# Optimization experiments

Measured on AMD Instinct MI355X. Metric: run time of the kernel, lower is better.

## Reference

```python
import jax, jax.numpy as jnp
import numpy as np

VERY_NEG = -1e30


def setup_inputs() -> dict:
    key = jax.random.key(0)
    k1, k2, k3, k4, k5 = jax.random.split(key, 5)
    T, J, B, D = 1024, 128, 32, 256
    context = jax.random.normal(k1, (T, B, D), dtype=jnp.float32)
    question = jax.random.normal(k2, (J, B, D), dtype=jnp.float32)
    con_lens = jax.random.randint(k3, (B,), 1, T + 1)
    qu_lens = jax.random.randint(k4, (B,), 1, J + 1)
    # learned trilinear weight (3*D, 1), small init like uniform weight init
    att_w = jax.random.normal(k5, (3 * D, 1), dtype=jnp.float32) * 0.05
    return {"context": context, "question": question, "con_lens": con_lens,
            "qu_lens": qu_lens, "att_w": att_w}


def reference(context, question, con_lens, qu_lens, att_w):
    T, B, D = context.shape
    J = question.shape[0]
    # Decompose trilinear score: [c, q, c*q] @ att_w = c.w_c + q.w_q + (c*q).w_cq
    w_c, w_q, w_cq = att_w[:D, 0], att_w[D:2 * D, 0], att_w[2 * D:, 0]
    c_proj = jnp.einsum('tbd,d->bt', context, w_c)            # (B,T)
    q_proj = jnp.einsum('jbd,d->bj', question, w_q)           # (B,J)
    cross = jnp.einsum('tbd,jbd->btj', context * w_cq, question)  # (B,T,J)
    S = c_proj[:, :, None] + q_proj[:, None, :] + cross       # (B,T,J)
    # exp_mask: valid (t < con_len) & (j < qu_len), invalid += VERY_NEG
    t_valid = jnp.arange(T)[None, :] < con_lens[:, None]      # (B,T)
    j_valid = jnp.arange(J)[None, :] < qu_lens[:, None]       # (B,J)
    valid = t_valid[:, :, None] & j_valid[:, None, :]         # (B,T,J)
    S = S + jnp.where(valid, 0.0, VERY_NEG)
    # context-to-query attention
    c2q_w = jax.nn.softmax(S, axis=-1)                        # (B,T,J)
    question_bt = jnp.transpose(question, (1, 0, 2))          # (B,J,D)
    c2q = jnp.einsum('btj,bjd->btd', c2q_w, question_bt)      # (B,T,D)
    # query-to-context attention: rows of the expanded bmm are identical,
    # so compute the weighted sum once and broadcast (same math as expand+bmm)
    value = jax.nn.softmax(jnp.max(S, axis=2), axis=-1)       # (B,T)
    context_bt = jnp.transpose(context, (1, 0, 2))            # (B,T,D)
    q2c_vec = jnp.einsum('bt,btd->bd', value, context_bt)     # (B,D)
    q2c = jnp.broadcast_to(q2c_vec[:, None, :], (B, T, D))
    G = jnp.concatenate([context_bt, c2q, context_bt * c2q, context_bt * q2c],
                        axis=2)                               # (B,T,4D)
    # zero out padded context positions
    G = G * t_valid[:, :, None].astype(G.dtype)
    return G
```

## Files before the change

kernel.cpp:

```cpp
#include <hip/hip_runtime.h>
#include <hip/hip_bf16.h>

#define T_ 1024
#define J_ 128
#define B_ 32
#define D_ 256
#define VERY_NEG (-1e30f)

using u16 = unsigned short;
typedef __bf16 bf16x8 __attribute__((ext_vector_type(8)));
typedef u16 u16x4 __attribute__((ext_vector_type(4)));
typedef float f32x4 __attribute__((ext_vector_type(4)));

__device__ __forceinline__ float bf2f(u16 u) {
  union { unsigned int i; float f; } v; v.i = ((unsigned int)u) << 16; return v.f;
}
__device__ __forceinline__ u16 f2bf(float f) {
  union { float f; unsigned int i; } v; v.f = f;
  unsigned int i = v.i;
  return (u16)((i + 0x7fffu + ((i >> 16) & 1u)) >> 16);
}

__global__ __launch_bounds__(256) void k_qproj(const float* __restrict__ qst,
                                               const float* __restrict__ attw,
                                               float* __restrict__ ws_qproj) {
  const int wave = threadIdx.x >> 6, lane = threadIdx.x & 63;
  const int gid = blockIdx.x * 4 + wave;
  const int b = gid >> 7, j = gid & 127;
  const float* src = qst + (size_t)j * (B_ * D_) + b * D_ + lane * 4;
  f32x4 a = *(const f32x4*)src;
  f32x4 w = *(const f32x4*)(attw + D_ + lane * 4);
  float s = a[0] * w[0] + a[1] * w[1] + a[2] * w[2] + a[3] * w[3];
#pragma unroll
  for (int m = 32; m >= 1; m >>= 1) s += __shfl_xor(s, m);
  if (lane == 0) ws_qproj[gid] = s;
}

__global__ __launch_bounds__(256) void k_main(const float* __restrict__ ctx,
                                              const float* __restrict__ qst,
                                              const int* __restrict__ con_lens,
                                              const int* __restrict__ qu_lens,
                                              const float* __restrict__ attw,
                                              const float* __restrict__ ws_qproj,
                                              float* __restrict__ ws_mrow,
                                              float* __restrict__ out) {
  __shared__ __align__(16) u16 smem[24576];
  u16* qtl = smem;
  u16* plds = smem + 16384;
  u16* c2q_l = smem;

  const int tid = threadIdx.x;
  const int wave = tid >> 6, lane = tid & 63;
  const int lrow = lane & 15, lgrp = lane >> 4;
  const int b = blockIdx.y;
  const int t0 = blockIdx.x * 64;
  const int t0w = t0 + wave * 16;
  const int con = con_lens[b], qu = qu_lens[b];

  f32x4 accS[8];
#pragma unroll
  for (int jb = 0; jb < 8; ++jb) accS[jb] = f32x4{0.f, 0.f, 0.f, 0.f};

  float cpr = 0.f;
  const float* rowAp = ctx + (size_t)(t0w + lrow) * (B_ * D_) + b * D_;
#pragma unroll
  for (int ks = 0; ks < 8; ++ks) {
    const int d0 = ks * 32 + lgrp * 8;
    f32x4 a0 = *(const f32x4*)(rowAp + d0);
    f32x4 a1 = *(const f32x4*)(rowAp + d0 + 4);
    f32x4 wq0 = *(const f32x4*)(attw + 2 * D_ + d0);
    f32x4 wq1 = *(const f32x4*)(attw + 2 * D_ + d0 + 4);
    f32x4 wc0 = *(const f32x4*)(attw + d0);
    f32x4 wc1 = *(const f32x4*)(attw + d0 + 4);
    bf16x8 afrag;
#pragma unroll
    for (int e = 0; e < 4; ++e) {
      afrag[e] = (__bf16)(a0[e] * wq0[e]);
      afrag[4 + e] = (__bf16)(a1[e] * wq1[e]);
      cpr += a0[e] * wc0[e] + a1[e] * wc1[e];
    }
#pragma unroll
    for (int jb = 0; jb < 8; ++jb) {
      const float* rb = qst + (size_t)(jb * 16 + lrow) * (B_ * D_) + b * D_ + d0;
      f32x4 b0 = *(const f32x4*)(rb);
      f32x4 b1 = *(const f32x4*)(rb + 4);
      bf16x8 bfrag;
#pragma unroll
      for (int e = 0; e < 4; ++e) {
        bfrag[e] = (__bf16)b0[e];
        bfrag[4 + e] = (__bf16)b1[e];
      }
      accS[jb] = __builtin_amdgcn_mfma_f32_16x16x32_bf16(afrag, bfrag, accS[jb], 0, 0, 0);
    }
  }
  cpr += __shfl_xor(cpr, 16);
  cpr += __shfl_xor(cpr, 32);

  float cp[4];
#pragma unroll
  for (int r = 0; r < 4; ++r) cp[r] = __shfl(cpr, lgrp * 4 + r);
  float qp[8];
#pragma unroll
  for (int jb = 0; jb < 8; ++jb) qp[jb] = ws_qproj[b * 128 + jb * 16 + lrow];

  float mx[4] = {-3e38f, -3e38f, -3e38f, -3e38f};
#pragma unroll
  for (int jb = 0; jb < 8; ++jb) {
    const int j = jb * 16 + lrow;
#pragma unroll
    for (int r = 0; r < 4; ++r) {
      const int t = t0w + lgrp * 4 + r;
      float s = accS[jb][r] + cp[r] + qp[jb];
      if (t >= con || j >= qu) s += VERY_NEG;
      accS[jb][r] = s;
      mx[r] = fmaxf(mx[r], s);
    }
  }
#pragma unroll
  for (int r = 0; r < 4; ++r) {
    mx[r] = fmaxf(mx[r], __shfl_xor(mx[r], 1));
    mx[r] = fmaxf(mx[r], __shfl_xor(mx[r], 2));
    mx[r] = fmaxf(mx[r], __shfl_xor(mx[r], 4));
    mx[r] = fmaxf(mx[r], __shfl_xor(mx[r], 8));
  }
  if (lrow == 0) {
#pragma unroll
    for (int r = 0; r < 4; ++r) ws_mrow[b * 1024 + t0w + lgrp * 4 + r] = mx[r];
  }
  float sm[4] = {0.f, 0.f, 0.f, 0.f};
#pragma unroll
  for (int jb = 0; jb < 8; ++jb)
#pragma unroll
    for (int r = 0; r < 4; ++r) {
      float p = __expf(accS[jb][r] - mx[r]);
      accS[jb][r] = p;
      sm[r] += p;
    }
#pragma unroll
  for (int r = 0; r < 4; ++r) {
    sm[r] += __shfl_xor(sm[r], 1);
    sm[r] += __shfl_xor(sm[r], 2);
    sm[r] += __shfl_xor(sm[r], 4);
    sm[r] += __shfl_xor(sm[r], 8);
  }

  {
    u16* pl = plds + wave * 2048;
#pragma unroll
    for (int r = 0; r < 4; ++r) {
      const float inv = 1.0f / sm[r];
      const int m = lgrp * 4 + r;
#pragma unroll
      for (int jb = 0; jb < 8; ++jb) {
        const int n = jb * 16 + lrow;
        pl[m * 128 + (((n >> 3) ^ m) << 3) + (n & 7)] = f2bf(accS[jb][r] * inv);
      }
    }
  }

  f32x4 accO[16];
#pragma unroll
  for (int nb = 0; nb < 16; ++nb) accO[nb] = f32x4{0.f, 0.f, 0.f, 0.f};

#pragma unroll
  for (int h = 0; h < 2; ++h) {
    __syncthreads();
    for (int it = 0; it < 8; ++it) {
      const int task = it * 256 + tid;
      const int j = task & 127, dblk = task >> 7;
      const float* qp8 = qst + (size_t)j * (B_ * D_) + b * D_ + h * 128 + dblk * 8;
      f32x4 q0 = *(const f32x4*)(qp8);
      f32x4 q1 = *(const f32x4*)(qp8 + 4);
#pragma unroll
      for (int e = 0; e < 8; ++e) {
        const int dl = dblk * 8 + e;
        const float v = (e < 4) ? q0[e] : q1[e - 4];
        qtl[dl * 128 + (((j >> 3) ^ (dl & 15)) << 3) + (j & 7)] = f2bf(v);
      }
    }
    __syncthreads();
#pragma unroll
    for (int ks2 = 0; ks2 < 4; ++ks2) {
      const int chunkA = ks2 * 4 + lgrp;
      const bf16x8 ap =
          *(const bf16x8*)(plds + wave * 2048 + lrow * 128 + ((chunkA ^ lrow) << 3));
#pragma unroll
      for (int nbl = 0; nbl < 8; ++nbl) {
        const int dl = nbl * 16 + lrow;
        const bf16x8 bq = *(const bf16x8*)(qtl + dl * 128 + ((chunkA ^ (dl & 15)) << 3));
        accO[h * 8 + nbl] =
            __builtin_amdgcn_mfma_f32_16x16x32_bf16(ap, bq, accO[h * 8 + nbl], 0, 0, 0);
      }
    }
  }
  __syncthreads();

#pragma unroll
  for (int nb = 0; nb < 16; ++nb)
#pragma unroll
    for (int r = 0; r < 4; ++r) {
      const int row = wave * 16 + lgrp * 4 + r;
      const int d = nb * 16 + lrow;
      c2q_l[row * 264 + d] = f2bf(accO[nb][r]);
    }
  __syncthreads();

  for (int ii = 0; ii < 16; ++ii) {
    const int idx = ii * 256 + tid;
    const int row = idx >> 6, c = idx & 63;
    const int t = t0 + row;
    const bool valid = t < con;
    f32x4 cr = *(const f32x4*)(ctx + (size_t)t * (B_ * D_) + b * D_ + c * 4);
    u16x4 cq = *(const u16x4*)(c2q_l + row * 264 + c * 4);
    f32x4 p0, p1, p2;
#pragma unroll
    for (int e = 0; e < 4; ++e) {
      const float cf = valid ? cr[e] : 0.f;
      const float qf = valid ? bf2f(cq[e]) : 0.f;
      p0[e] = cf;
      p1[e] = qf;
      p2[e] = cf * qf;
    }
    float* g = out + ((size_t)(b * 1024 + t)) * 1024 + c * 4;
    *(f32x4*)(g) = p0;
    *(f32x4*)(g + 256) = p1;
    *(f32x4*)(g + 512) = p2;
  }
}

__global__ __launch_bounds__(256) void k_value(const float* __restrict__ ctx,
                                               const float* __restrict__ mrow,
                                               float* __restrict__ q2c) {
  __shared__ float wls[1024];
  __shared__ float red[8];
  const int b = blockIdx.x >> 3, tc = blockIdx.x & 7;
  const int tid = threadIdx.x;
  const int wave = tid >> 6, lane = tid & 63;
  const float* mr = mrow + b * 1024;

  float mx = -3e38f;
  for (int t = tid; t < 1024; t += 256) mx = fmaxf(mx, mr[t]);
#pragma unroll
  for (int m = 32; m >= 1; m >>= 1) mx = fmaxf(mx, __shfl_xor(mx, m));
  if (lane == 0) red[wave] = mx;
  __syncthreads();
  mx = fmaxf(fmaxf(red[0], red[1]), fmaxf(red[2], red[3]));

  float sl = 0.f;
  for (int t = tid; t < 1024; t += 256) {
    float wv = __expf(mr[t] - mx);
    wls[t] = wv;
    sl += wv;
  }
#pragma unroll
  for (int m = 32; m >= 1; m >>= 1) sl += __shfl_xor(sl, m);
  if (lane == 0) red[4 + wave] = sl;
  __syncthreads();
  const float inv = 1.0f / (red[4] + red[5] + red[6] + red[7]);

  const int d = tid;
  const float* cp = ctx + b * D_ + d;
  const int tb = tc * 128;
  float a0 = 0.f, a1 = 0.f, a2 = 0.f, a3 = 0.f;
  for (int t = tb; t < tb + 128; t += 4) {
    a0 += wls[t + 0] * cp[(size_t)(t + 0) * (B_ * D_)];
    a1 += wls[t + 1] * cp[(size_t)(t + 1) * (B_ * D_)];
    a2 += wls[t + 2] * cp[(size_t)(t + 2) * (B_ * D_)];
    a3 += wls[t + 3] * cp[(size_t)(t + 3) * (B_ * D_)];
  }
  atomicAdd(&q2c[b * D_ + d], (a0 + a1 + a2 + a3) * inv);
}

__global__ __launch_bounds__(256) void k_part3(const float* __restrict__ ctx,
                                               const int* __restrict__ con_lens,
                                               const float* __restrict__ q2c,
                                               float* __restrict__ out) {
  const int idx = blockIdx.x * 256 + threadIdx.x;
  const int c = idx & 63, t = (idx >> 6) & 1023, b = idx >> 16;
  const bool valid = t < con_lens[b];
  f32x4 cr = *(const f32x4*)(ctx + (size_t)t * (B_ * D_) + b * D_ + c * 4);
  const f32x4 qv = *(const f32x4*)(q2c + b * D_ + c * 4);
  f32x4 o;
#pragma unroll
  for (int e = 0; e < 4; ++e) o[e] = valid ? cr[e] * qv[e] : 0.f;
  *(f32x4*)(out + ((size_t)(b * 1024 + t)) * 1024 + 768 + c * 4) = o;
}

extern "C" void kernel_launch(void* const* d_in, const int* in_sizes, int n_in,
                              void* d_out, int out_size, void* d_ws, size_t ws_size,
                              hipStream_t stream) {
  const float* ctx = (const float*)d_in[0];
  const float* qst = (const float*)d_in[1];
  const int* con = (const int*)d_in[2];
  const int* qu = (const int*)d_in[3];
  const float* attw = (const float*)d_in[4];
  float* out = (float*)d_out;

  float* ws = (float*)d_ws;
  float* ws_qproj = ws;
  float* ws_mrow = ws + 4096;
  float* ws_q2c = ws + 36864;

  hipMemsetAsync((void*)ws_q2c, 0, B_ * D_ * sizeof(float), stream);
  k_qproj<<<1024, 256, 0, stream>>>(qst, attw, ws_qproj);
  k_main<<<dim3(16, 32), 256, 0, stream>>>(ctx, qst, con, qu, attw, ws_qproj, ws_mrow,
                                           out);
  k_value<<<256, 256, 0, stream>>>(ctx, ws_mrow, ws_q2c);
  k_part3<<<8192, 256, 0, stream>>>(ctx, con, ws_q2c, out);
}
```

Measured before the change: 218.9 us.

## Fuse q2c softmax partials into main kernel and precast question to bf16

```diff
diff --git a/kernel.cpp b/kernel.cpp
--- a/kernel.cpp
+++ b/kernel.cpp
@@ -9,6 +9,7 @@
 
 using u16 = unsigned short;
 typedef __bf16 bf16x8 __attribute__((ext_vector_type(8)));
+typedef u16 u16x8 __attribute__((ext_vector_type(8)));
 typedef u16 u16x4 __attribute__((ext_vector_type(4)));
 typedef float f32x4 __attribute__((ext_vector_type(4)));
 
@@ -21,15 +22,20 @@
   return (u16)((i + 0x7fffu + ((i >> 16) & 1u)) >> 16);
 }
 
-__global__ __launch_bounds__(256) void k_qproj(const float* __restrict__ qst,
-                                               const float* __restrict__ attw,
-                                               float* __restrict__ ws_qproj) {
+__global__ __launch_bounds__(256) void k_prep(const float* __restrict__ qst,
+                                              const float* __restrict__ attw,
+                                              float* __restrict__ ws_qproj,
+                                              u16* __restrict__ ws_qbf) {
   const int wave = threadIdx.x >> 6, lane = threadIdx.x & 63;
   const int gid = blockIdx.x * 4 + wave;
   const int b = gid >> 7, j = gid & 127;
-  const float* src = qst + (size_t)j * (B_ * D_) + b * D_ + lane * 4;
-  f32x4 a = *(const f32x4*)src;
+  const size_t off = (size_t)j * (B_ * D_) + b * D_ + lane * 4;
+  f32x4 a = *(const f32x4*)(qst + off);
   f32x4 w = *(const f32x4*)(attw + D_ + lane * 4);
+  u16x4 qb;
+#pragma unroll
+  for (int e = 0; e < 4; ++e) qb[e] = f2bf(a[e]);
+  *(u16x4*)(ws_qbf + off) = qb;
   float s = a[0] * w[0] + a[1] * w[1] + a[2] * w[2] + a[3] * w[3];
 #pragma unroll
   for (int m = 32; m >= 1; m >>= 1) s += __shfl_xor(s, m);
@@ -37,17 +43,22 @@
 }
 
 __global__ __launch_bounds__(256) void k_main(const float* __restrict__ ctx,
-                                              const float* __restrict__ qst,
+                                              const u16* __restrict__ qbf,
                                               const int* __restrict__ con_lens,
                                               const int* __restrict__ qu_lens,
                                               const float* __restrict__ attw,
                                               const float* __restrict__ ws_qproj,
-                                              float* __restrict__ ws_mrow,
+                                              float* __restrict__ ws_mtile,
+                                              float* __restrict__ ws_pden,
+                                              float* __restrict__ ws_pnum,
                                               float* __restrict__ out) {
   __shared__ __align__(16) u16 smem[24576];
+  __shared__ float mrow_l[64];
+  __shared__ float msc[1];
   u16* qtl = smem;
   u16* plds = smem + 16384;
   u16* c2q_l = smem;
+  float* red4 = (float*)(smem + 16896);
 
   const int tid = threadIdx.x;
   const int wave = tid >> 6, lane = tid & 63;
@@ -81,15 +92,8 @@
     }
 #pragma unroll
     for (int jb = 0; jb < 8; ++jb) {
-      const float* rb = qst + (size_t)(jb * 16 + lrow) * (B_ * D_) + b * D_ + d0;
-      f32x4 b0 = *(const f32x4*)(rb);
-      f32x4 b1 = *(const f32x4*)(rb + 4);
-      bf16x8 bfrag;
-#pragma unroll
-      for (int e = 0; e < 4; ++e) {
-        bfrag[e] = (__bf16)b0[e];
-        bfrag[4 + e] = (__bf16)b1[e];
-      }
+      const bf16x8 bfrag =
+          *(const bf16x8*)(qbf + (size_t)(jb * 16 + lrow) * (B_ * D_) + b * D_ + d0);
       accS[jb] = __builtin_amdgcn_mfma_f32_16x16x32_bf16(afrag, bfrag, accS[jb], 0, 0, 0);
     }
   }
@@ -125,7 +129,7 @@
   }
   if (lrow == 0) {
 #pragma unroll
-    for (int r = 0; r < 4; ++r) ws_mrow[b * 1024 + t0w + lgrp * 4 + r] = mx[r];
+    for (int r = 0; r < 4; ++r) mrow_l[wave * 16 + lgrp * 4 + r] = mx[r];
   }
   float sm[4] = {0.f, 0.f, 0.f, 0.f};
 #pragma unroll
@@ -168,14 +172,11 @@
     for (int it = 0; it < 8; ++it) {
       const int task = it * 256 + tid;
       const int j = task & 127, dblk = task >> 7;
-      const float* qp8 = qst + (size_t)j * (B_ * D_) + b * D_ + h * 128 + dblk * 8;
-      f32x4 q0 = *(const f32x4*)(qp8);
-      f32x4 q1 = *(const f32x4*)(qp8 + 4);
+      u16x8 q = *(const u16x8*)(qbf + (size_t)j * (B_ * D_) + b * D_ + h * 128 + dblk * 8);
 #pragma unroll
       for (int e = 0; e < 8; ++e) {
         const int dl = dblk * 8 + e;
-        const float v = (e < 4) ? q0[e] : q1[e - 4];
-        qtl[dl * 128 + (((j >> 3) ^ (dl & 15)) << 3) + (j & 7)] = f2bf(v);
+        qtl[dl * 128 + (((j >> 3) ^ (dl & 15)) << 3) + (j & 7)] = q[e];
       }
     }
     __syncthreads();
@@ -205,13 +206,37 @@
     }
   __syncthreads();
 
+  if (tid < 64) {
+    float v = mrow_l[tid];
+#pragma unroll
+    for (int m = 32; m >= 1; m >>= 1) v = fmaxf(v, __shfl_xor(v, m));
+    if (tid == 0) msc[0] = v;
+  }
+  __syncthreads();
+  const float Mt = msc[0];
+  if (tid < 64) {
+    const float mr = mrow_l[tid];
+    const float e = (mr < -1e29f) ? 0.f : __expf(mr - Mt);
+    mrow_l[tid] = e;
+    float s2 = e;
+#pragma unroll
+    for (int m = 32; m >= 1; m >>= 1) s2 += __shfl_xor(s2, m);
+    if (tid == 0) {
+      ws_mtile[b * 16 + blockIdx.x] = Mt;
+      ws_pden[b * 16 + blockIdx.x] = s2;
+    }
+  }
+  __syncthreads();
+
+  f32x4 acc4 = {0.f, 0.f, 0.f, 0.f};
+  const int c = tid & 63;
   for (int ii = 0; ii < 16; ++ii) {
-    const int idx = ii * 256 + tid;
-    const int row = idx >> 6, c = idx & 63;
+    const int row = ii * 4 + wave;
     const int t = t0 + row;
     const bool valid = t < con;
     f32x4 cr = *(const f32x4*)(ctx + (size_t)t * (B_ * D_) + b * D_ + c * 4);
     u16x4 cq = *(const u16x4*)(c2q_l + row * 264 + c * 4);
+    const float w = mrow_l[row];
     f32x4 p0, p1, p2;
 #pragma unroll
     for (int e = 0; e < 4; ++e) {
@@ -220,55 +245,47 @@
       p0[e] = cf;
       p1[e] = qf;
       p2[e] = cf * qf;
+      acc4[e] += w * cr[e];
     }
     float* g = out + ((size_t)(b * 1024 + t)) * 1024 + c * 4;
     *(f32x4*)(g) = p0;
     *(f32x4*)(g + 256) = p1;
     *(f32x4*)(g + 512) = p2;
   }
-}
-
-__global__ __launch_bounds__(256) void k_value(const float* __restrict__ ctx,
-                                               const float* __restrict__ mrow,
-                                               float* __restrict__ q2c) {
-  __shared__ float wls[1024];
-  __shared__ float red[8];
-  const int b = blockIdx.x >> 3, tc = blockIdx.x & 7;
-  const int tid = threadIdx.x;
-  const int wave = tid >> 6, lane = tid & 63;
-  const float* mr = mrow + b * 1024;
-
-  float mx = -3e38f;
-  for (int t = tid; t < 1024; t += 256) mx = fmaxf(mx, mr[t]);
-#pragma unroll
-  for (int m = 32; m >= 1; m >>= 1) mx = fmaxf(mx, __shfl_xor(mx, m));
-  if (lane == 0) red[wave] = mx;
-  __syncthreads();
-  mx = fmaxf(fmaxf(red[0], red[1]), fmaxf(red[2], red[3]));
-
-  float sl = 0.f;
-  for (int t = tid; t < 1024; t += 256) {
-    float wv = __expf(mr[t] - mx);
-    wls[t] = wv;
-    sl += wv;
-  }
-#pragma unroll
-  for (int m = 32; m >= 1; m >>= 1) sl += __shfl_xor(sl, m);
-  if (lane == 0) red[4 + wave] = sl;
-  __syncthreads();
-  const float inv = 1.0f / (red[4] + red[5] + red[6] + red[7]);
-
-  const int d = tid;
-  const float* cp = ctx + b * D_ + d;
-  const int tb = tc * 128;
-  float a0 = 0.f, a1 = 0.f, a2 = 0.f, a3 = 0.f;
-  for (int t = tb; t < tb + 128; t += 4) {
-    a0 += wls[t + 0] * cp[(size_t)(t + 0) * (B_ * D_)];
-    a1 += wls[t + 1] * cp[(size_t)(t + 1) * (B_ * D_)];
-    a2 += wls[t + 2] * cp[(size_t)(t + 2) * (B_ * D_)];
-    a3 += wls[t + 3] * cp[(size_t)(t + 3) * (B_ * D_)];
-  }
-  atomicAdd(&q2c[b * D_ + d], (a0 + a1 + a2 + a3) * inv);
+  *(f32x4*)(red4 + wave * 256 + c * 4) = acc4;
+  __syncthreads();
+  {
+    const float sum = red4[tid] + red4[256 + tid] + red4[512 + tid] + red4[768 + tid];
+    ws_pnum[((size_t)b * 16 + blockIdx.x) * 256 + tid] = sum;
+  }
+}
+
+__global__ __launch_bounds__(256) void k_combine(const float* __restrict__ ws_mtile,
+                                                 const float* __restrict__ ws_pden,
+                                                 const float* __restrict__ ws_pnum,
+                                                 float* __restrict__ q2c) {
+  __shared__ float se[16];
+  __shared__ float sden[1];
+  const int b = blockIdx.x, tid = threadIdx.x;
+  if (tid < 64) {
+    const float mt = (tid < 16) ? ws_mtile[b * 16 + tid] : -3e38f;
+    float M = mt;
+#pragma unroll
+    for (int m = 8; m >= 1; m >>= 1) M = fmaxf(M, __shfl_xor(M, m));
+    const float pd = (tid < 16) ? ws_pden[b * 16 + tid] : 0.f;
+    const float e = (tid < 16 && mt > -1e29f) ? __expf(mt - M) : 0.f;
+    if (tid < 16) se[tid] = e;
+    float cden = e * pd;
+#pragma unroll
+    for (int m = 8; m >= 1; m >>= 1) cden += __shfl_xor(cden, m);
+    if (tid == 0) sden[0] = cden;
+  }
+  __syncthreads();
+  const float den = sden[0];
+  float num = 0.f;
+#pragma unroll
+  for (int i = 0; i < 16; ++i) num += se[i] * ws_pnum[((size_t)b * 16 + i) * 256 + tid];
+  q2c[b * 256 + tid] = num / den;
 }
 
 __global__ __launch_bounds__(256) void k_part3(const float* __restrict__ ctx,
@@ -298,13 +315,15 @@
 
   float* ws = (float*)d_ws;
   float* ws_qproj = ws;
-  float* ws_mrow = ws + 4096;
-  float* ws_q2c = ws + 36864;
-
-  hipMemsetAsync((void*)ws_q2c, 0, B_ * D_ * sizeof(float), stream);
-  k_qproj<<<1024, 256, 0, stream>>>(qst, attw, ws_qproj);
-  k_main<<<dim3(16, 32), 256, 0, stream>>>(ctx, qst, con, qu, attw, ws_qproj, ws_mrow,
-                                           out);
-  k_value<<<256, 256, 0, stream>>>(ctx, ws_mrow, ws_q2c);
+  u16* ws_qbf = (u16*)(ws + 4096);
+  float* ws_mtile = ws + 528384;
+  float* ws_pden = ws + 528896;
+  float* ws_pnum = ws + 529408;
+  float* ws_q2c = ws + 660480;
+
+  k_prep<<<1024, 256, 0, stream>>>(qst, attw, ws_qproj, ws_qbf);
+  k_main<<<dim3(16, 32), 256, 0, stream>>>(ctx, ws_qbf, con, qu, attw, ws_qproj,
+                                           ws_mtile, ws_pden, ws_pnum, out);
+  k_combine<<<32, 256, 0, stream>>>(ws_mtile, ws_pden, ws_pnum, ws_q2c);
   k_part3<<<8192, 256, 0, stream>>>(ctx, con, ws_q2c, out);
 }
```

Measured after the change: 190.7 us. 12.9% less time.
